# Optimization experiments

Hardware: AMD Instinct MI355X
Metric: run time of the kernel (lower is better)

The kernel has to match this reference:

```python
import jax, jax.numpy as jnp
import numpy as np

D_MODEL, HIDDEN, N_EXPERTS, TOP_K = 1024, 2048, 8, 2
RMS_EPS = 1e-6


def setup_inputs() -> dict:
    key = jax.random.key(0)
    ks = jax.random.split(key, 6)
    B, S = 4, 2048
    return {
        "x": jax.random.normal(ks[0], (B, S, D_MODEL), jnp.float32),
        "norm_weight": jnp.ones((D_MODEL,), jnp.float32),
        "gate_w": jax.random.normal(ks[1], (N_EXPERTS, D_MODEL), jnp.float32) * 0.02,
        "w1": jax.random.normal(ks[2], (N_EXPERTS, HIDDEN, D_MODEL), jnp.float32) * 0.02,
        "b1": jnp.zeros((N_EXPERTS, HIDDEN), jnp.float32),
        "w2": jax.random.normal(ks[3], (N_EXPERTS, D_MODEL, HIDDEN), jnp.float32) * 0.02,
        "b2": jnp.zeros((N_EXPERTS, D_MODEL), jnp.float32),
    }


def reference(x, norm_weight, gate_w, w1, b1, w2, b2):
    B, S, D = x.shape
    E = gate_w.shape[0]
    # RMSNorm
    t = x * jax.lax.rsqrt(jnp.mean(x * x, axis=-1, keepdims=True) + RMS_EPS) * norm_weight
    tokens = t.reshape(-1, D)                      # [T, D]
    T = tokens.shape[0]
    # Top-k routing (eval mode: no gate noise)
    gate_logits = tokens @ gate_w.T                # [T, E]
    gate_scores, expert_idx = jax.lax.top_k(gate_logits, TOP_K)
    routing_weights = jax.nn.softmax(gate_scores, axis=-1)  # [T, K]
    # Per-token per-expert combine weight (scatter routing weights into [T, E])
    combine = jnp.zeros((T, E), tokens.dtype).at[
        jnp.arange(T)[:, None], expert_idx
    ].add(routing_weights)
    # Scan over experts; inactive tokens have combine weight 0, matching the
    # masked gather/scatter-add math of the original exactly.
    def body(acc, params):
        W1, B1, W2, B2, c = params                 # c: [T]
        h = jax.nn.gelu(tokens @ W1.T + B1, approximate=False)  # [T, H]
        o = h @ W2.T + B2                          # [T, D]
        return acc + c[:, None] * o, None

    out, _ = jax.lax.scan(body, jnp.zeros_like(tokens), (w1, b1, w2, b2, combine.T))
    return x + out.reshape(B, S, D)
```

## Files before the change

### kernel.cpp

```cpp
#include <hip/hip_runtime.h>
#include <hip/hip_bf16.h>
#include <stdint.h>

#define D_MODEL 1024
#define HIDDEN  2048
#define N_EXP   8
#define T_TOK   8192
#define MAXPOS  17408
#define ROWTILES (MAXPOS/128)

typedef __attribute__((ext_vector_type(4))) float f32x4;
typedef __attribute__((ext_vector_type(8))) short short8v;

__device__ __forceinline__ unsigned short f2bf(float f) {
    union { float f; unsigned int u; } v; v.f = f;
    unsigned int u = v.u;
    unsigned int r = (u + 0x7fffu + ((u >> 16) & 1u)) >> 16;
    return (unsigned short)r;
}

__device__ __forceinline__ void gload_lds16(const void* g, void* l) {
    __builtin_amdgcn_global_load_lds(
        reinterpret_cast<const __attribute__((address_space(1))) unsigned int*>(
            reinterpret_cast<uintptr_t>(g)),
        reinterpret_cast<__attribute__((address_space(3))) unsigned int*>(
            (uint32_t)reinterpret_cast<uintptr_t>(l)),
        16, 0, 0);
}

__global__ void rms_gate_kernel(const float* __restrict__ x,
                                const float* __restrict__ nw,
                                const float* __restrict__ gw,
                                unsigned short* __restrict__ tb,
                                int* __restrict__ tok_e,
                                float* __restrict__ tok_w) {
    const int wave = threadIdx.x >> 6;
    const int lane = threadIdx.x & 63;
    const int t = blockIdx.x * 4 + wave;

    const float4* xr = (const float4*)(x + (size_t)t * D_MODEL);
    const float4* wr = (const float4*)nw;
    float4 xv[4], wv[4];
    #pragma unroll
    for (int j = 0; j < 4; j++) {
        xv[j] = xr[j * 64 + lane];
        wv[j] = wr[j * 64 + lane];
    }

    float ssq = 0.0f;
    #pragma unroll
    for (int j = 0; j < 4; j++)
        ssq += xv[j].x * xv[j].x + xv[j].y * xv[j].y + xv[j].z * xv[j].z + xv[j].w * xv[j].w;
    #pragma unroll
    for (int off = 32; off; off >>= 1) ssq += __shfl_xor(ssq, off);
    const float scale = rsqrtf(ssq * (1.0f / D_MODEL) + 1e-6f);

    float4 tn[4];
    #pragma unroll
    for (int j = 0; j < 4; j++) {
        tn[j].x = xv[j].x * wv[j].x * scale;
        tn[j].y = xv[j].y * wv[j].y * scale;
        tn[j].z = xv[j].z * wv[j].z * scale;
        tn[j].w = xv[j].w * wv[j].w * scale;
    }

    ushort4* tw = (ushort4*)(tb + (size_t)t * D_MODEL);
    #pragma unroll
    for (int j = 0; j < 4; j++) {
        ushort4 o;
        o.x = f2bf(tn[j].x); o.y = f2bf(tn[j].y);
        o.z = f2bf(tn[j].z); o.w = f2bf(tn[j].w);
        tw[j * 64 + lane] = o;
    }

    float d[8];
    #pragma unroll
    for (int e = 0; e < 8; e++) {
        d[e] = 0.0f;
        #pragma unroll
        for (int j = 0; j < 4; j++) {
            float4 g = ((const float4*)(gw + e * D_MODEL))[j * 64 + lane];
            d[e] += tn[j].x * g.x + tn[j].y * g.y + tn[j].z * g.z + tn[j].w * g.w;
        }
    }
    #pragma unroll
    for (int e = 0; e < 8; e++) {
        #pragma unroll
        for (int off = 32; off; off >>= 1) d[e] += __shfl_xor(d[e], off);
    }

    if (lane == 0) {
        int i0 = 0;
        #pragma unroll
        for (int e = 1; e < 8; e++) if (d[e] > d[i0]) i0 = e;
        int i1 = -1;
        #pragma unroll
        for (int e = 0; e < 8; e++)
            if (e != i0 && (i1 < 0 || d[e] > d[i1])) i1 = e;
        float e1 = expf(d[i1] - d[i0]);
        float w0 = 1.0f / (1.0f + e1);
        ((int2*)tok_e)[t]   = make_int2(i0, i1);
        ((float2*)tok_w)[t] = make_float2(w0, e1 * w0);
    }
}

__global__ void hist_kernel(const int* __restrict__ tok_e, int* __restrict__ counts) {
    __shared__ int lh[8];
    if (threadIdx.x < 8) lh[threadIdx.x] = 0;
    __syncthreads();
    int i = blockIdx.x * 512 + threadIdx.x;
    atomicAdd(&lh[tok_e[i]], 1);
    atomicAdd(&lh[tok_e[i + 256]], 1);
    __syncthreads();
    if (threadIdx.x < 8) atomicAdd(&counts[threadIdx.x], lh[threadIdx.x]);
}

__global__ void scan_fill_kernel(int* __restrict__ perm_tok, float* __restrict__ perm_w,
                                 const int* __restrict__ counts,
                                 int* __restrict__ poff, int* __restrict__ pos_ctr) {
    int i = blockIdx.x * 256 + threadIdx.x;
    if (i < MAXPOS) { perm_tok[i] = 0; perm_w[i] = 0.0f; }
    if (blockIdx.x == 0 && threadIdx.x == 0) {
        int acc = 0; poff[0] = 0;
        #pragma unroll
        for (int e = 0; e < 8; e++) {
            pos_ctr[e] = 0;
            acc += (counts[e] + 127) & ~127;
            poff[e + 1] = acc;
        }
    }
}

__global__ void scatter_kernel(const int* __restrict__ tok_e, const float* __restrict__ tok_w,
                               const int* __restrict__ poff, int* __restrict__ pos_ctr,
                               int* __restrict__ perm_tok, float* __restrict__ perm_w) {
    __shared__ int lh[8], lbase[8];
    if (threadIdx.x < 8) lh[threadIdx.x] = 0;
    __syncthreads();
    int t = blockIdx.x * 256 + threadIdx.x;
    int2   ee = ((const int2*)tok_e)[t];
    float2 ww = ((const float2*)tok_w)[t];
    int p0 = atomicAdd(&lh[ee.x], 1);
    int p1 = atomicAdd(&lh[ee.y], 1);
    __syncthreads();
    if (threadIdx.x < 8) lbase[threadIdx.x] = atomicAdd(&pos_ctr[threadIdx.x], lh[threadIdx.x]);
    __syncthreads();
    int q0 = poff[ee.x] + lbase[ee.x] + p0;
    int q1 = poff[ee.y] + lbase[ee.y] + p1;
    perm_tok[q0] = t; perm_w[q0] = ww.x;
    perm_tok[q1] = t; perm_w[q1] = ww.y;
}

__global__ void cvt_bf16_kernel(const float4* __restrict__ in,
                                ushort4* __restrict__ outp, int n4) {
    int i = blockIdx.x * blockDim.x + threadIdx.x;
    if (i >= n4) return;
    float4 v = in[i];
    ushort4 o; o.x = f2bf(v.x); o.y = f2bf(v.y); o.z = f2bf(v.z); o.w = f2bf(v.w);
    outp[i] = o;
}

template <int MODE, int K, int N>
__global__ void moe_gemm_kernel(const unsigned short* __restrict__ A,
                                const unsigned short* __restrict__ W,
                                const float* __restrict__ bias,
                                const int* __restrict__ perm_tok,
                                const float* __restrict__ perm_w,
                                const int* __restrict__ poff,
                                unsigned short* __restrict__ Hout,
                                float* __restrict__ Out) {
    constexpr int NT = N / 128;
    __shared__ short lds[2 * 128 * 64];
    short* Asm = lds;
    short* Bsm = lds + 128 * 64;

    const int nwg = gridDim.x;
    const int cpx = nwg >> 3;
    const int bid = (int)blockIdx.x;
    const int swz = (bid & 7) * cpx + (bid >> 3);

    const int rt = swz / NT, nt = swz % NT;
    const int row_base = rt * 128;
    if (row_base >= poff[8]) return;
    int e = 0;
    while (poff[e + 1] <= row_base) ++e;
    const int n0 = nt * 128;

    const int tid = threadIdx.x;
    const int wave = tid >> 6, lane = tid & 63;
    const int colb = (tid & 7) * 16;
    const int wr = wave >> 1, wc = wave & 1;

    size_t aoff[4], boff[4];
    #pragma unroll
    for (int i = 0; i < 4; i++) {
        int r = row_base + i * 32 + (tid >> 3);
        int arow = (MODE == 1) ? perm_tok[r] : r;
        aoff[i] = (size_t)arow * (K * 2);
        int brow = n0 + i * 32 + (tid >> 3);
        boff[i] = ((size_t)e * N + brow) * (size_t)(K * 2);
    }
    const char* Ab = (const char*)A;
    const char* Wb = (const char*)W;

    f32x4 acc[4][4];
    #pragma unroll
    for (int mi = 0; mi < 4; mi++)
        #pragma unroll
        for (int ni = 0; ni < 4; ni++) acc[mi][ni] = (f32x4)(0.0f);

    for (int k0b = 0; k0b < K * 2; k0b += 128) {
        #pragma unroll
        for (int i = 0; i < 4; i++) {
            gload_lds16(Ab + aoff[i] + k0b + colb, (char*)Asm + i * 4096 + wave * 1024);
            gload_lds16(Wb + boff[i] + k0b + colb, (char*)Bsm + i * 4096 + wave * 1024);
        }
        __syncthreads();
        #pragma unroll
        for (int kk = 0; kk < 2; kk++) {
            short8v af[4], bf[4];
            #pragma unroll
            for (int mi = 0; mi < 4; mi++)
                af[mi] = *(const short8v*)&Asm[(wr * 64 + mi * 16 + (lane & 15)) * 64 + kk * 32 + (lane >> 4) * 8];
            #pragma unroll
            for (int ni = 0; ni < 4; ni++)
                bf[ni] = *(const short8v*)&Bsm[(wc * 64 + ni * 16 + (lane & 15)) * 64 + kk * 32 + (lane >> 4) * 8];
            #pragma unroll
            for (int mi = 0; mi < 4; mi++)
                #pragma unroll
                for (int ni = 0; ni < 4; ni++)
                    acc[mi][ni] = __builtin_amdgcn_mfma_f32_16x16x32_bf16(af[mi], bf[ni], acc[mi][ni], 0, 0, 0);
        }
        __syncthreads();
    }

    if (MODE == 1) {
        #pragma unroll
        for (int mi = 0; mi < 4; mi++) {
            #pragma unroll
            for (int ni = 0; ni < 4; ni++) {
                int c = n0 + wc * 64 + ni * 16 + (lane & 15);
                float bv = bias[e * N + c];
                #pragma unroll
                for (int j = 0; j < 4; j++) {
                    int r = row_base + wr * 64 + mi * 16 + (lane >> 4) * 4 + j;
                    float v = acc[mi][ni][j] + bv;
                    v = 0.5f * v * (1.0f + erff(v * 0.70710678118654752f));
                    Hout[(size_t)r * N + c] = f2bf(v);
                }
            }
        }
    } else {
        #pragma unroll
        for (int mi = 0; mi < 4; mi++) {
            #pragma unroll
            for (int j = 0; j < 4; j++) {
                int r = row_base + wr * 64 + mi * 16 + (lane >> 4) * 4 + j;
                float wgt = perm_w[r];
                if (wgt != 0.0f) {
                    int tok = perm_tok[r];
                    float* orow = Out + (size_t)tok * N;
                    #pragma unroll
                    for (int ni = 0; ni < 4; ni++) {
                        int c = n0 + wc * 64 + ni * 16 + (lane & 15);
                        atomicAdd(&orow[c], wgt * (acc[mi][ni][j] + bias[e * N + c]));
                    }
                }
            }
        }
    }
}

extern "C" void kernel_launch(void* const* d_in, const int* in_sizes, int n_in,
                              void* d_out, int out_size, void* d_ws, size_t ws_size,
                              hipStream_t stream) {
    const float* x  = (const float*)d_in[0];
    const float* nw = (const float*)d_in[1];
    const float* gw = (const float*)d_in[2];
    const float* w1 = (const float*)d_in[3];
    const float* b1 = (const float*)d_in[4];
    const float* w2 = (const float*)d_in[5];
    const float* b2 = (const float*)d_in[6];
    float* out = (float*)d_out;
    char* ws = (char*)d_ws;

    size_t off = 0;
    unsigned short* tb  = (unsigned short*)(ws + off); off += (size_t)T_TOK * D_MODEL * 2;
    unsigned short* w1b = (unsigned short*)(ws + off); off += (size_t)N_EXP * HIDDEN * D_MODEL * 2;
    unsigned short* w2b = (unsigned short*)(ws + off); off += (size_t)N_EXP * D_MODEL * HIDDEN * 2;
    unsigned short* h   = (unsigned short*)(ws + off); off += (size_t)MAXPOS * HIDDEN * 2;
    int*   perm_tok = (int*)(ws + off);   off += MAXPOS * 4;
    float* perm_w   = (float*)(ws + off); off += MAXPOS * 4;
    int*   tok_e    = (int*)(ws + off);   off += T_TOK * 2 * 4;
    float* tok_w    = (float*)(ws + off); off += T_TOK * 2 * 4;
    int*   meta     = (int*)(ws + off);
    int* counts  = meta;
    int* pos_ctr = meta + 8;
    int* poff    = meta + 16;

    hipMemsetAsync(meta, 0, 32, stream);
    hipMemcpyAsync(out, x, (size_t)T_TOK * D_MODEL * 4,
                   hipMemcpyDeviceToDevice, stream);

    rms_gate_kernel<<<T_TOK / 4, 256, 0, stream>>>(x, nw, gw, tb, tok_e, tok_w);

    const int n4 = N_EXP * HIDDEN * D_MODEL / 4;
    cvt_bf16_kernel<<<n4 / 256, 256, 0, stream>>>((const float4*)w1, (ushort4*)w1b, n4);
    cvt_bf16_kernel<<<n4 / 256, 256, 0, stream>>>((const float4*)w2, (ushort4*)w2b, n4);

    hist_kernel<<<32, 256, 0, stream>>>(tok_e, counts);
    scan_fill_kernel<<<MAXPOS / 256, 256, 0, stream>>>(perm_tok, perm_w, counts, poff, pos_ctr);
    scatter_kernel<<<T_TOK / 256, 256, 0, stream>>>(tok_e, tok_w, poff, pos_ctr, perm_tok, perm_w);

    moe_gemm_kernel<1, D_MODEL, HIDDEN><<<ROWTILES * (HIDDEN / 128), 256, 0, stream>>>(
        tb, w1b, b1, perm_tok, perm_w, poff, h, nullptr);
    moe_gemm_kernel<2, HIDDEN, D_MODEL><<<ROWTILES * (D_MODEL / 128), 256, 0, stream>>>(
        h, w2b, b2, perm_tok, perm_w, poff, nullptr, out);
}
```

Baseline: 356.9 us.

## Fuse residual copy into RMS kernel, merge weight casts, stage GEMM1 output via LDS

The residual copy of x into the output moves into the RMSNorm/gate kernel, which already reads x, so the separate device-to-device memcpy and its extra read of x go away. The two weight bf16 conversion launches become one kernel. The first GEMM epilogue now writes GELU results into LDS and then issues coalesced 16-byte row stores to H instead of scattered 2-byte stores, at the cost of extra barriers. A launch-bounds annotation is also added to the GEMM.

```diff
diff --git a/kernel.cpp b/kernel.cpp
--- a/kernel.cpp
+++ b/kernel.cpp
@@ -33,19 +33,23 @@
                                 const float* __restrict__ gw,
                                 unsigned short* __restrict__ tb,
                                 int* __restrict__ tok_e,
-                                float* __restrict__ tok_w) {
+                                float* __restrict__ tok_w,
+                                float* __restrict__ out) {
     const int wave = threadIdx.x >> 6;
     const int lane = threadIdx.x & 63;
     const int t = blockIdx.x * 4 + wave;
 
     const float4* xr = (const float4*)(x + (size_t)t * D_MODEL);
     const float4* wr = (const float4*)nw;
+    float4* orow = (float4*)(out + (size_t)t * D_MODEL);
     float4 xv[4], wv[4];
     #pragma unroll
     for (int j = 0; j < 4; j++) {
         xv[j] = xr[j * 64 + lane];
         wv[j] = wr[j * 64 + lane];
     }
+    #pragma unroll
+    for (int j = 0; j < 4; j++) orow[j * 64 + lane] = xv[j];
 
     float ssq = 0.0f;
     #pragma unroll
@@ -151,17 +155,21 @@
     perm_tok[q1] = t; perm_w[q1] = ww.y;
 }
 
-__global__ void cvt_bf16_kernel(const float4* __restrict__ in,
-                                ushort4* __restrict__ outp, int n4) {
-    int i = blockIdx.x * blockDim.x + threadIdx.x;
-    if (i >= n4) return;
-    float4 v = in[i];
+__global__ void cvt2_bf16_kernel(const float4* __restrict__ a, ushort4* __restrict__ ao,
+                                 const float4* __restrict__ b, ushort4* __restrict__ bo,
+                                 int n4) {
+    int i = blockIdx.x * 256 + threadIdx.x;
+    const float4* src = (i < n4) ? a : b;
+    ushort4* dst = (i < n4) ? ao : bo;
+    int idx = (i < n4) ? i : i - n4;
+    float4 v = src[idx];
     ushort4 o; o.x = f2bf(v.x); o.y = f2bf(v.y); o.z = f2bf(v.z); o.w = f2bf(v.w);
-    outp[i] = o;
+    dst[idx] = o;
 }
 
 template <int MODE, int K, int N>
-__global__ void moe_gemm_kernel(const unsigned short* __restrict__ A,
+__global__ __launch_bounds__(256) void moe_gemm_kernel(
+                                const unsigned short* __restrict__ A,
                                 const unsigned short* __restrict__ W,
                                 const float* __restrict__ bias,
                                 const int* __restrict__ perm_tok,
@@ -236,19 +244,36 @@
 
     if (MODE == 1) {
         #pragma unroll
-        for (int mi = 0; mi < 4; mi++) {
-            #pragma unroll
-            for (int ni = 0; ni < 4; ni++) {
-                int c = n0 + wc * 64 + ni * 16 + (lane & 15);
-                float bv = bias[e * N + c];
+        for (int hh = 0; hh < 2; hh++) {
+            if (wr == hh) {
                 #pragma unroll
-                for (int j = 0; j < 4; j++) {
-                    int r = row_base + wr * 64 + mi * 16 + (lane >> 4) * 4 + j;
-                    float v = acc[mi][ni][j] + bv;
-                    v = 0.5f * v * (1.0f + erff(v * 0.70710678118654752f));
-                    Hout[(size_t)r * N + c] = f2bf(v);
+                for (int mi = 0; mi < 4; mi++) {
+                    #pragma unroll
+                    for (int ni = 0; ni < 4; ni++) {
+                        int lc = wc * 64 + ni * 16 + (lane & 15);
+                        float bv = bias[e * N + n0 + lc];
+                        #pragma unroll
+                        for (int j = 0; j < 4; j++) {
+                            int lr = mi * 16 + (lane >> 4) * 4 + j;
+                            float v = acc[mi][ni][j] + bv;
+                            v = 0.5f * v * (1.0f + erff(v * 0.70710678118654752f));
+                            lds[lr * 136 + lc] = (short)f2bf(v);
+                        }
+                    }
                 }
             }
+            __syncthreads();
+            {
+                const int rr = tid >> 4;
+                const int cc = tid & 15;
+                #pragma unroll
+                for (int p = 0; p < 4; p++) {
+                    int lr = p * 16 + rr;
+                    short8v v = *(const short8v*)&lds[lr * 136 + cc * 8];
+                    *(short8v*)(Hout + (size_t)(row_base + hh * 64 + lr) * N + n0 + cc * 8) = v;
+                }
+            }
+            __syncthreads();
         }
     } else {
         #pragma unroll
@@ -299,14 +324,12 @@
     int* poff    = meta + 16;
 
     hipMemsetAsync(meta, 0, 32, stream);
-    hipMemcpyAsync(out, x, (size_t)T_TOK * D_MODEL * 4,
-                   hipMemcpyDeviceToDevice, stream);
-
-    rms_gate_kernel<<<T_TOK / 4, 256, 0, stream>>>(x, nw, gw, tb, tok_e, tok_w);
+
+    rms_gate_kernel<<<T_TOK / 4, 256, 0, stream>>>(x, nw, gw, tb, tok_e, tok_w, out);
 
     const int n4 = N_EXP * HIDDEN * D_MODEL / 4;
-    cvt_bf16_kernel<<<n4 / 256, 256, 0, stream>>>((const float4*)w1, (ushort4*)w1b, n4);
-    cvt_bf16_kernel<<<n4 / 256, 256, 0, stream>>>((const float4*)w2, (ushort4*)w2b, n4);
+    cvt2_bf16_kernel<<<2 * n4 / 256, 256, 0, stream>>>(
+        (const float4*)w1, (ushort4*)w1b, (const float4*)w2, (ushort4*)w2b, n4);
 
     hist_kernel<<<32, 256, 0, stream>>>(tok_e, counts);
     scan_fill_kernel<<<MAXPOS / 256, 256, 0, stream>>>(perm_tok, perm_w, counts, poff, pos_ctr);
```

Result: slower. 497.0 us (+39.3%).
